# Kernel tuning notes

Hardware: AMD Instinct MI355X
Metric: run time of the kernel (lower is better)

The kernel has to match this reference:

```python
import jax, jax.numpy as jnp
import numpy as np

N, L, S, C, H = 4, 2048, 4096, 256, 8
D = C // H          # head dim = 32
HID = 4 * C         # mlp hidden = 1024
LN_EPS = 1e-5
LA_EPS = 1e-6


def _layer_norm(x, g, b):
    m = x.mean(-1, keepdims=True)
    v = ((x - m) ** 2).mean(-1, keepdims=True)
    return (x - m) * jax.lax.rsqrt(v + LN_EPS) * g + b


def _linear_attention(q, k, v):
    # q: [N,L,H,D], k/v: [N,S,H,D]  (elu feature map linear attention)
    Q = jax.nn.elu(q) + 1.0
    K = jax.nn.elu(k) + 1.0
    v_len = v.shape[1]
    KV = jnp.einsum('nshd,nshv->nhdv', K, v / v_len)
    Z = 1.0 / (jnp.einsum('nlhd,nhd->nlh', Q, K.sum(axis=1)) + LA_EPS)
    return jnp.einsum('nlhd,nhdv,nlh->nlhv', Q, KV, Z) * v_len


def setup_inputs() -> dict:
    key = jax.random.key(0)
    ks = jax.random.split(key, 32)
    f32 = jnp.float32
    w = lambda k, *s: (jax.random.normal(k, s, dtype=f32) * 0.02)
    inp = {
        'tgt': jax.random.normal(ks[0], (N, L, C), dtype=f32),
        'memory': jax.random.normal(ks[1], (N, S, C), dtype=f32),
        'tgt_pos': jax.random.normal(ks[2], (N, L, C), dtype=f32),
        'pos_embed': w(ks[3], 1, S, C),
        # layer norms
        'ln1_g': jnp.ones((C,), f32), 'ln1_b': jnp.zeros((C,), f32),
        'ln2_g': jnp.ones((C,), f32), 'ln2_b': jnp.zeros((C,), f32),
        'ln3_g': jnp.ones((C,), f32), 'ln3_b': jnp.zeros((C,), f32),
        # self-attn projections (stored (in,out))
        'wq': w(ks[4], C, C), 'bq': jnp.zeros((C,), f32),
        'wk': w(ks[5], C, C), 'bk': jnp.zeros((C,), f32),
        'wv': w(ks[6], C, C), 'bv': jnp.zeros((C,), f32),
        'w_merge': w(ks[7], C, C),
        # cross-attn (CCAttention) projections
        'cwq': w(ks[8], C, C), 'cbq': jnp.zeros((C,), f32),
        'cwk': w(ks[9], C, C), 'cbk': jnp.zeros((C,), f32),
        'cwv': w(ks[10], C, C), 'cbv': jnp.zeros((C,), f32),
        'cwo': w(ks[11], C, C), 'cbo': jnp.zeros((C,), f32),
        # mlp (fc1 -> dwconv3x3 -> gelu -> fc2)
        'mw1': w(ks[12], C, HID), 'mb1': jnp.zeros((HID,), f32),
        'dw_k': w(ks[13], HID, 1, 3, 3), 'dw_b': jnp.zeros((HID,), f32),
        'mw2': w(ks[14], HID, C), 'mb2': jnp.zeros((C,), f32),
        'num_points': L,
    }
    return inp


def reference(tgt, memory, tgt_pos, pos_embed,
              ln1_g, ln1_b, ln2_g, ln2_b, ln3_g, ln3_b,
              wq, bq, wk, bk, wv, bv, w_merge,
              cwq, cbq, cwk, cbk, cwv, cbv, cwo, cbo,
              mw1, mb1, dw_k, dw_b, mw2, mb2, num_points):
    n, l, c = tgt.shape
    # ---- self attention (linear attention) ----
    tgt2 = _layer_norm(tgt, ln1_g, ln1_b)
    qk = tgt2 + tgt_pos
    q = (qk @ wq + bq).reshape(n, l, H, D)
    k = (qk @ wk + bk).reshape(n, l, H, D)
    v = (tgt2 @ wv + bv).reshape(n, l, H, D)
    msg = _linear_attention(q, k, v).reshape(n, l, c) @ w_merge
    tgt = tgt + msg  # dropout is identity in eval
    # ---- cross attention (CCAttention, softmax MHA) ----
    tgt2 = _layer_norm(tgt, ln2_g, ln2_b)
    mem = memory + pos_embed
    cq = (tgt2 @ cwq + cbq).reshape(n, l, H, D)
    ck = (mem @ cwk + cbk).reshape(n, -1, H, D)
    cv = (mem @ cwv + cbv).reshape(n, -1, H, D)
    scale = D ** -0.5
    attn = jax.nn.softmax(jnp.einsum('nlhd,nshd->nhls', cq, ck) * scale, axis=-1)
    cmsg = jnp.einsum('nhls,nshd->nlhd', attn, cv).reshape(n, l, c) @ cwo + cbo
    tgt = tgt + cmsg
    # ---- MLP with depthwise conv over (num_points, 1) grid ----
    x = _layer_norm(tgt, ln3_g, ln3_b)
    h = x @ mw1 + mb1                                   # [n,l,HID]
    hi = h.transpose(0, 2, 1).reshape(n, HID, num_points, 1)
    hi = jax.lax.conv_general_dilated(
        hi, dw_k, window_strides=(1, 1), padding=((1, 1), (1, 1)),
        feature_group_count=HID,
        dimension_numbers=('NCHW', 'OIHW', 'NCHW'))
    hi = hi + dw_b[None, :, None, None]
    h = hi.reshape(n, HID, l).transpose(0, 2, 1)
    h = jax.nn.gelu(h, approximate=False)
    mlp_out = h @ mw2 + mb2
    return tgt + mlp_out
```

## Files before the change

### kernel.cpp

```cpp
#include <hip/hip_runtime.h>
#include <hip/hip_bf16.h>
#include <math.h>

#define NB 4
#define LL 2048
#define SS 4096
#define CC 256
#define HH 8
#define DD 32
#define HIDN 1024
#define NSPLIT 4

using bf16 = __hip_bfloat16;
typedef __attribute__((ext_vector_type(8))) short short8;
typedef __attribute__((ext_vector_type(4))) short short4v;
typedef __attribute__((ext_vector_type(4))) float floatx4;

__device__ __forceinline__ float b2f(bf16 x) { return __bfloat162float(x); }
__device__ __forceinline__ short f2bs(float x) {
    bf16 h = __float2bfloat16(x);
    return *(short*)&h;
}
__device__ __forceinline__ short f2bs_fast(float x) {
    return (short)(__float_as_uint(x) >> 16);
}
__device__ __forceinline__ float s2f(short s) {
    bf16 h = *(bf16*)&s;
    return __bfloat162float(h);
}

#if __has_builtin(__builtin_amdgcn_exp2f)
#define EXP2(x) __builtin_amdgcn_exp2f(x)
#else
#define EXP2(x) exp2f(x)
#endif

__device__ __forceinline__ bool probe_f32(const unsigned* p) {
    return p[0] == 0x3F800000u;
}
__device__ __forceinline__ float ldx(const void* p, size_t i, bool f32m) {
    return f32m ? ((const float*)p)[i] : b2f(((const bf16*)p)[i]);
}

struct WPack { const void* p[10]; };

__global__ __launch_bounds__(256)
void wprep_kernel(WPack pk, short* __restrict__ dst, float* __restrict__ zbuf,
                  const unsigned* __restrict__ probe) {
    const int z = blockIdx.z;
    const int tid = threadIdx.x;
    if (z == 10) {
        int idx = (blockIdx.y * 16 + blockIdx.x) * 256 + tid;
        if (idx < 35072) zbuf[idx] = 0.0f;
        return;
    }
    const bool f32m = probe_f32(probe);
    const int K = (z == 9) ? 1024 : 256;
    const int N = (z == 8) ? 1024 : 256;
    const size_t off = (z < 8) ? (size_t)z * 65536 : (z == 8 ? 524288u : 786432u);
    const int k0 = blockIdx.y * 64, n0 = blockIdx.x * 64;
    if (k0 >= K || n0 >= N) return;
    __shared__ float T[64][65];
    const void* src = pk.p[z];
    #pragma unroll
    for (int p = 0; p < 16; ++p) {
        int idx = tid + p * 256;
        int r = idx >> 6, c = idx & 63;
        T[r][c] = ldx(src, (size_t)(k0 + r) * N + n0 + c, f32m);
    }
    __syncthreads();
    short* d = dst + off;
    #pragma unroll
    for (int p = 0; p < 16; ++p) {
        int idx = tid + p * 256;
        int c2 = idx >> 6, r2 = idx & 63;
        d[(size_t)(n0 + c2) * K + k0 + r2] = f2bs(T[r2][c2]);
    }
}

__global__ __launch_bounds__(256)
void ln_kernel(const void* __restrict__ xr, const float* __restrict__ xf,
               const void* __restrict__ g, const void* __restrict__ bta,
               const void* __restrict__ pos,
               short* __restrict__ y, short* __restrict__ y2,
               const unsigned* __restrict__ probe) {
    const bool f32m = probe_f32(probe);
    const int row = blockIdx.x;
    const int c = threadIdx.x;
    const size_t base = (size_t)row * CC;
    float x = xr ? ldx(xr, base + c, f32m) : xf[base + c];
    float a = x, b = x * x;
    #pragma unroll
    for (int off = 32; off; off >>= 1) {
        a += __shfl_down(a, off);
        b += __shfl_down(b, off);
    }
    __shared__ float sa[4], sb[4];
    if ((c & 63) == 0) { sa[c >> 6] = a; sb[c >> 6] = b; }
    __syncthreads();
    float s1 = sa[0] + sa[1] + sa[2] + sa[3];
    float s2 = sb[0] + sb[1] + sb[2] + sb[3];
    float mean = s1 * (1.0f / CC);
    float var = s2 * (1.0f / CC) - mean * mean;
    float inv = rsqrtf(var + 1e-5f);
    float yv = (x - mean) * inv * ldx(g, c, f32m) + ldx(bta, c, f32m);
    y[base + c] = f2bs(yv);
    if (y2) y2[base + c] = f2bs(yv + ldx(pos, base + c, f32m));
}

__global__ __launch_bounds__(256)
void ln_addpos_kernel(const float* __restrict__ xf, const void* __restrict__ g,
                      const void* __restrict__ bta, short* __restrict__ y,
                      const void* __restrict__ mem, const void* __restrict__ pos,
                      short* __restrict__ memout,
                      const unsigned* __restrict__ probe) {
    const bool f32m = probe_f32(probe);
    int row = blockIdx.x;
    const int c = threadIdx.x;
    if (row >= NB * LL) {
        row -= NB * LL;
        const int s = row & (SS - 1);
        memout[(size_t)row * CC + c] =
            f2bs(ldx(mem, (size_t)row * CC + c, f32m) + ldx(pos, (size_t)s * CC + c, f32m));
        return;
    }
    const size_t base = (size_t)row * CC;
    float x = xf[base + c];
    float a = x, b = x * x;
    #pragma unroll
    for (int off = 32; off; off >>= 1) {
        a += __shfl_down(a, off);
        b += __shfl_down(b, off);
    }
    __shared__ float sa[4], sb[4];
    if ((c & 63) == 0) { sa[c >> 6] = a; sb[c >> 6] = b; }
    __syncthreads();
    float s1 = sa[0] + sa[1] + sa[2] + sa[3];
    float s2 = sb[0] + sb[1] + sb[2] + sb[3];
    float mean = s1 * (1.0f / CC);
    float var = s2 * (1.0f / CC) - mean * mean;
    float inv = rsqrtf(var + 1e-5f);
    y[base + c] = f2bs((x - mean) * inv * ldx(g, c, f32m) + ldx(bta, c, f32m));
}

template <int BM, int BN>
__device__ __forceinline__
void gemm_body(const short* __restrict__ A, const short* __restrict__ Bt,
               const void* bias, const void* bias2,
               const float* __restrict__ residF, const void* __restrict__ residR,
               void* Cout, void* Cout2,
               int N, int K, bool f32m, int epi, int outmode, int transc2,
               int bx, int by) {
    constexpr int WM = BM / 2, AI = WM / 16;
    constexpr int WN = BN / 2, BJ = WN / 16;
    constexpr int ACH = (BM == 128) ? 4 : 2;
    constexpr int BCH = (BN == 128) ? 4 : 2;
    __shared__ __attribute__((aligned(16))) short As[BM][72];
    __shared__ __attribute__((aligned(16))) short Bs[BN][72];
    const int tid = threadIdx.x;
    const int ln = tid & 15, quad = (tid >> 4) & 3, w = tid >> 6;
    const int wm = (w & 1) * WM, wn = (w >> 1) * WN;
    const int bm = by * BM, bn = bx * BN;
    const int ar = (BM == 128) ? (tid >> 1) : (tid >> 2);
    const int ac = (BM == 128) ? ((tid & 1) * 32) : ((tid & 3) * 16);
    const int br = (BN == 128) ? (tid >> 1) : (tid >> 2);
    const int bc = (BN == 128) ? ((tid & 1) * 32) : ((tid & 3) * 16);

    short8 pa[ACH], pb[BCH];
    {
        const short* ag = &A[(size_t)(bm + ar) * K + ac];
        #pragma unroll
        for (int t = 0; t < ACH; ++t) pa[t] = *(const short8*)(ag + t * 8);
        const short* bg = &Bt[(size_t)(bn + br) * K + bc];
        #pragma unroll
        for (int t = 0; t < BCH; ++t) pb[t] = *(const short8*)(bg + t * 8);
    }
    floatx4 acc[AI][BJ] = {};
    for (int k0 = 0; k0 < K; k0 += 64) {
        #pragma unroll
        for (int t = 0; t < ACH; ++t) *(short8*)&As[ar][ac + t * 8] = pa[t];
        #pragma unroll
        for (int t = 0; t < BCH; ++t) *(short8*)&Bs[br][bc + t * 8] = pb[t];
        if (k0 + 64 < K) {
            const short* ag = &A[(size_t)(bm + ar) * K + k0 + 64 + ac];
            #pragma unroll
            for (int t = 0; t < ACH; ++t) pa[t] = *(const short8*)(ag + t * 8);
            const short* bg = &Bt[(size_t)(bn + br) * K + k0 + 64 + bc];
            #pragma unroll
            for (int t = 0; t < BCH; ++t) pb[t] = *(const short8*)(bg + t * 8);
        }
        __syncthreads();
        #pragma unroll
        for (int ks = 0; ks < 2; ++ks) {
            short8 af[AI], bf[BJ];
            #pragma unroll
            for (int i = 0; i < AI; ++i)
                af[i] = *(const short8*)&As[wm + i * 16 + ln][ks * 32 + quad * 8];
            #pragma unroll
            for (int j = 0; j < BJ; ++j)
                bf[j] = *(const short8*)&Bs[wn + j * 16 + ln][ks * 32 + quad * 8];
            #pragma unroll
            for (int i = 0; i < AI; ++i)
                #pragma unroll
                for (int j = 0; j < BJ; ++j)
                    acc[i][j] = __builtin_amdgcn_mfma_f32_16x16x32_bf16(af[i], bf[j], acc[i][j], 0, 0, 0);
        }
        __syncthreads();
    }
    #pragma unroll
    for (int i = 0; i < AI; ++i)
        #pragma unroll
        for (int j = 0; j < BJ; ++j) {
            const int gr0 = bm + wm + i * 16 + quad * 4;
            const int gc = bn + wn + j * 16 + ln;
            const bool hi = (Cout2 != nullptr) && (gc >= 256);
            const int col = hi ? gc - 256 : gc;
            const int sN = Cout2 ? 256 : N;
            void* co = hi ? Cout2 : Cout;
            const void* bb = hi ? bias2 : bias;
            float vv[4];
            #pragma unroll
            for (int r = 0; r < 4; ++r) {
                float v = acc[i][j][r];
                if (bb) v += ldx(bb, col, f32m);
                if (epi == 1) v = (v > 0.0f) ? (v + 1.0f) : __expf(v);
                const size_t o = (size_t)(gr0 + r) * sN + col;
                if (residF) v += residF[o];
                if (residR) v += ldx(residR, o, f32m);
                vv[r] = v;
            }
            if (transc2 && hi) {
                const int nb = gr0 >> 12;
                const int s = gr0 & (SS - 1);
                short4v pk4 = {f2bs(vv[0]), f2bs(vv[1]), f2bs(vv[2]), f2bs(vv[3])};
                *(short4v*)&((short*)co)[((size_t)nb * CC + col) * SS + s] = pk4;
            } else {
                #pragma unroll
                for (int r = 0; r < 4; ++r) {
                    const size_t o = (size_t)(gr0 + r) * sN + col;
                    if (outmode == 0) ((float*)co)[o] = vv[r];
                    else if (outmode == 2) ((short*)co)[o] = f2bs(vv[r]);
                    else {
                        if (f32m) ((float*)co)[o] = vv[r];
                        else      ((bf16*)co)[o] = __float2bfloat16(vv[r]);
                    }
                }
            }
        }
}

template <int BM, int BN, int EPI, int OUTMODE, int TRANSC2>
__global__ __launch_bounds__(256)
void gemm_mfma_kernel(const short* __restrict__ A, const short* __restrict__ Bt,
                      const void* __restrict__ bias, const void* __restrict__ bias2,
                      const float* __restrict__ residF, const void* __restrict__ residR,
                      void* __restrict__ Cout, void* __restrict__ Cout2,
                      int M, int N, int K, const unsigned* __restrict__ probe) {
    (void)M;
    gemm_body<BM, BN>(A, Bt, bias, bias2, residF, residR, Cout, Cout2,
                      N, K, probe_f32(probe), EPI, OUTMODE, TRANSC2,
                      blockIdx.x, blockIdx.y);
}

__global__ __launch_bounds__(256)
void gemm_qkv_kernel(const short* __restrict__ qkA, const short* __restrict__ wqkT,
                     const void* bq, const void* bk,
                     float* __restrict__ phiq, float* __restrict__ phik,
                     const short* __restrict__ vA, const short* __restrict__ wvT,
                     const void* bv, float* __restrict__ vout,
                     const unsigned* __restrict__ probe) {
    const bool f32m = probe_f32(probe);
    const bool second = blockIdx.x >= 8;
    gemm_body<64, 64>(second ? vA : qkA,
                      second ? wvT : wqkT,
                      second ? bv : bq,
                      second ? nullptr : bk,
                      nullptr, nullptr,
                      second ? (void*)vout : (void*)phiq,
                      second ? nullptr : (void*)phik,
                      second ? 256 : 512, 256, f32m,
                      second ? 0 : 1, 0, 0,
                      second ? (int)blockIdx.x - 8 : (int)blockIdx.x, blockIdx.y);
}

__global__ __launch_bounds__(256)
void gemm_cqckcv_kernel(const short* __restrict__ lnA, const short* __restrict__ cwqT,
                        const void* cbq, short* __restrict__ cqout,
                        const short* __restrict__ memA, const short* __restrict__ cwkvT,
                        const void* cbk, const void* cbv,
                        short* __restrict__ ckout, short* __restrict__ cvTout,
                        const unsigned* __restrict__ probe) {
    const bool f32m = probe_f32(probe);
    const bool second = blockIdx.x >= 4;
    if (!second && blockIdx.y >= (NB * LL) / 64) return;
    gemm_body<64, 64>(second ? memA : lnA,
                      second ? cwkvT : cwqT,
                      second ? cbk : cbq,
                      second ? cbv : nullptr,
                      nullptr, nullptr,
                      second ? (void*)ckout : (void*)cqout,
                      second ? (void*)cvTout : nullptr,
                      second ? 512 : 256, 256, f32m,
                      0, 2, second ? 1 : 0,
                      second ? (int)blockIdx.x - 4 : (int)blockIdx.x, blockIdx.y);
}

#define KVSPLIT 16
__global__ __launch_bounds__(256)
void linattn_kv_kernel(const float* __restrict__ Kp, const float* __restrict__ Vp,
                       float* __restrict__ KV, float* __restrict__ Ksum) {
    const int h = blockIdx.x, n = blockIdx.y, z = blockIdx.z;
    __shared__ __attribute__((aligned(16))) float Kt[64][33];
    __shared__ __attribute__((aligned(16))) float Vt[64][32];
    const int tid = threadIdx.x;
    const int d = tid >> 3, e0 = (tid & 7) * 4;
    const int sbeg = z * (LL / KVSPLIT), send = sbeg + (LL / KVSPLIT);
    float acc[4] = {}, ks = 0.0f;
    for (int s0 = sbeg; s0 < send; s0 += 64) {
        #pragma unroll
        for (int p = 0; p < 8; ++p) {
            int idx = tid + p * 256;
            int r = idx >> 5, c = idx & 31;
            size_t gaddr = (size_t)((n * LL) + s0 + r) * CC + h * DD + c;
            Kt[r][c] = Kp[gaddr];
            Vt[r][c] = Vp[gaddr];
        }
        __syncthreads();
        for (int s = 0; s < 64; ++s) {
            float kd = Kt[s][d];
            ks += kd;
            float4 v4 = *(const float4*)&Vt[s][e0];
            acc[0] += kd * v4.x; acc[1] += kd * v4.y;
            acc[2] += kd * v4.z; acc[3] += kd * v4.w;
        }
        __syncthreads();
    }
    float* kvp = &KV[(size_t)((n * HH + h) * DD + d) * DD + e0];
    atomicAdd(&kvp[0], acc[0]); atomicAdd(&kvp[1], acc[1]);
    atomicAdd(&kvp[2], acc[2]); atomicAdd(&kvp[3], acc[3]);
    if ((tid & 7) == 0) atomicAdd(&Ksum[(n * HH + h) * DD + d], ks);
}

__global__ __launch_bounds__(256)
void linattn_out_kernel(const float* __restrict__ Qp, const float* __restrict__ KV,
                        const float* __restrict__ Ksum, short* __restrict__ Out) {
    const int lt = blockIdx.x, h = blockIdx.y, n = blockIdx.z;
    __shared__ float KVs[32][33];
    __shared__ float Ks[32];
    __shared__ float Qs[64][33];
    const int tid = threadIdx.x;
    for (int p = 0; p < 4; ++p) {
        int idx = tid + p * 256;
        KVs[idx >> 5][idx & 31] = KV[(size_t)(n * HH + h) * (DD * DD) + idx];
    }
    if (tid < 32) Ks[tid] = Ksum[(n * HH + h) * DD + tid];
    for (int p = 0; p < 8; ++p) {
        int idx = tid + p * 256;
        int r = idx >> 5, c = idx & 31;
        Qs[r][c] = Qp[(size_t)((n * LL) + lt * 64 + r) * CC + h * DD + c];
    }
    __syncthreads();
    const int e = tid & 31;
    for (int ii = 0; ii < 8; ++ii) {
        const int i = (tid >> 5) + ii * 8;
        float num = 0.0f, den = 0.0f;
        for (int d = 0; d < 32; ++d) {
            float q = Qs[i][d];
            num += q * KVs[d][e];
            den += q * Ks[d];
        }
        Out[(size_t)((n * LL) + lt * 64 + i) * CC + h * DD + e] = f2bs(num / (den + 1e-6f));
    }
}

__global__ __launch_bounds__(256)
void flash_mfma_kernel(const short* __restrict__ Q, const short* __restrict__ K,
                       const short* __restrict__ V,
                       float* __restrict__ Of, float* __restrict__ Lp) {
    const int lt = blockIdx.x, h = blockIdx.y;
    const int n = blockIdx.z / NSPLIT, sp = blockIdx.z % NSPLIT;
    const int tid = threadIdx.x;
    const int ln = tid & 15;
    const int quad = (tid >> 4) & 3;
    const int w = tid >> 6;
    const int NT = NB * LL;
    const float qscale = 0.17677669529663687f * 1.4426950408889634f;

    __shared__ __attribute__((aligned(16))) short Ks[2][64][40];
    __shared__ __attribute__((aligned(16))) short Vp[2][32][72];

    short8 bQa, bQb;
    {
        const size_t qrow = (size_t)(n * LL) + lt * 128 + w * 16 + ln;
        short8 qv0 = *(const short8*)&Q[qrow * CC + h * DD + quad * 8];
        short8 qv1 = *(const short8*)&Q[(qrow + 64) * CC + h * DD + quad * 8];
        short t0[8], t1[8];
        #pragma unroll
        for (int j = 0; j < 8; ++j) {
            t0[j] = f2bs(s2f(qv0[j]) * qscale);
            t1[j] = f2bs(s2f(qv1[j]) * qscale);
        }
        bQa = *(short8*)t0;
        bQb = *(short8*)t1;
    }

    const short one_b = (short)0x3F80;
    const short8 ones8 = {one_b, one_b, one_b, one_b, one_b, one_b, one_b, one_b};

    floatx4 o0a = {0.f, 0.f, 0.f, 0.f}, o1a = {0.f, 0.f, 0.f, 0.f};
    floatx4 o2a = {0.f, 0.f, 0.f, 0.f};
    floatx4 o0b = {0.f, 0.f, 0.f, 0.f}, o1b = {0.f, 0.f, 0.f, 0.f};
    floatx4 o2b = {0.f, 0.f, 0.f, 0.f};
    const floatx4 zinit = {-24.f, -24.f, -24.f, -24.f};

    const int r_st = tid >> 2, c0_st = (tid & 3) * 8;
    const int e_st = tid >> 3, m_st = tid & 7;
    const int K32 = (m_st >> 2) * 32;
    const int h4 = ((m_st >> 1) & 1) * 4;
    const int q0s = (2 * m_st) & 3;
    const int slotA = K32 + q0s * 8 + h4;
    const int slotB = K32 + (q0s + 1) * 8 + h4;

    const int sbeg = sp * (SS / NSPLIT);
    constexpr int NIT = (SS / NSPLIT) / 64;

    const short* kptr = &K[(size_t)((n * SS) + sbeg + r_st) * CC + h * DD + c0_st];
    const short* vptr = &V[((size_t)n * CC + h * DD + e_st) * SS + sbeg + m_st * 8];
    short8 kreg = *(const short8*)kptr;
    short8 vreg = *(const short8*)vptr;

    for (int it = 0; it < NIT; ++it) {
        const int buf = it & 1;
        *(short8*)&Ks[buf][r_st][c0_st] = kreg;
        {
            short4v lo = {vreg[0], vreg[1], vreg[2], vreg[3]};
            short4v hi = {vreg[4], vreg[5], vreg[6], vreg[7]};
            *(short4v*)&Vp[buf][e_st][slotA] = lo;
            *(short4v*)&Vp[buf][e_st][slotB] = hi;
        }
        if (it + 1 < NIT) {
            kreg = *(const short8*)(kptr + (size_t)(it + 1) * 64 * CC);
            vreg = *(const short8*)(vptr + (it + 1) * 64);
        }
        __syncthreads();

        floatx4 sa[4], sb[4];
        #pragma unroll
        for (int g = 0; g < 4; ++g) {
            short8 aK = *(const short8*)&Ks[buf][g * 16 + ln][quad * 8];
            sa[g] = __builtin_amdgcn_mfma_f32_16x16x32_bf16(aK, bQa, zinit, 0, 0, 0);
            sb[g] = __builtin_amdgcn_mfma_f32_16x16x32_bf16(aK, bQb, zinit, 0, 0, 0);
        }

        #pragma unroll
        for (int ks = 0; ks < 2; ++ks) {
            union { unsigned u[4]; short8 s8; } ca, cb;
            #pragma unroll
            for (int jj = 0; jj < 4; ++jj) {
                const int j0 = 2 * jj, j1 = 2 * jj + 1;
                float pa0 = EXP2(sa[2 * ks + (j0 >> 2)][j0 & 3]);
                float pa1 = EXP2(sa[2 * ks + (j1 >> 2)][j1 & 3]);
                ca.u[jj] = __builtin_amdgcn_perm(
                    __float_as_uint(pa1), __float_as_uint(pa0), 0x07060302u);
                float pb0 = EXP2(sb[2 * ks + (j0 >> 2)][j0 & 3]);
                float pb1 = EXP2(sb[2 * ks + (j1 >> 2)][j1 & 3]);
                cb.u[jj] = __builtin_amdgcn_perm(
                    __float_as_uint(pb1), __float_as_uint(pb0), 0x07060302u);
            }
            short8 bV0 = *(const short8*)&Vp[buf][ln][ks * 32 + quad * 8];
            short8 bV1 = *(const short8*)&Vp[buf][16 + ln][ks * 32 + quad * 8];
            o0a = __builtin_amdgcn_mfma_f32_16x16x32_bf16(ca.s8, bV0, o0a, 0, 0, 0);
            o1a = __builtin_amdgcn_mfma_f32_16x16x32_bf16(ca.s8, bV1, o1a, 0, 0, 0);
            o2a = __builtin_amdgcn_mfma_f32_16x16x32_bf16(ca.s8, ones8, o2a, 0, 0, 0);
            o0b = __builtin_amdgcn_mfma_f32_16x16x32_bf16(cb.s8, bV0, o0b, 0, 0, 0);
            o1b = __builtin_amdgcn_mfma_f32_16x16x32_bf16(cb.s8, bV1, o1b, 0, 0, 0);
            o2b = __builtin_amdgcn_mfma_f32_16x16x32_bf16(cb.s8, ones8, o2b, 0, 0, 0);
        }
    }

    const int rb_a = lt * 128 + w * 16;
    const int rb_b = rb_a + 64;
    if (ln == 0) {
        #pragma unroll
        for (int r = 0; r < 4; ++r) {
            Lp[((size_t)sp * NT + (size_t)n * LL + rb_a + quad * 4 + r) * HH + h] = o2a[r];
            Lp[((size_t)sp * NT + (size_t)n * LL + rb_b + quad * 4 + r) * HH + h] = o2b[r];
        }
    }
    #pragma unroll
    for (int r = 0; r < 4; ++r) {
        {
            const size_t row = (size_t)n * LL + rb_a + quad * 4 + r;
            float* o = &Of[((size_t)sp * NT + row) * CC + h * DD];
            o[ln] = o0a[r];
            o[16 + ln] = o1a[r];
        }
        {
            const size_t row = (size_t)n * LL + rb_b + quad * 4 + r;
            float* o = &Of[((size_t)sp * NT + row) * CC + h * DD];
            o[ln] = o0b[r];
            o[16 + ln] = o1b[r];
        }
    }
}

__global__ __launch_bounds__(256)
void flash_merge_kernel(const float* __restrict__ Of, const float* __restrict__ Lp,
                        short* __restrict__ O) {
    const int row = blockIdx.x, c = threadIdx.x, h = c >> 5;
    const size_t NT = (size_t)NB * LL;
    float l = 0.0f, v = 0.0f;
    #pragma unroll
    for (int sp = 0; sp < NSPLIT; ++sp) {
        l += Lp[((size_t)sp * NT + row) * HH + h];
        v += Of[((size_t)sp * NT + row) * CC + c];
    }
    O[(size_t)row * CC + c] = f2bs(v / l);
}

__global__ __launch_bounds__(256)
void dwconv_gelu_kernel(const short* __restrict__ H1, const void* __restrict__ wk,
                        const void* __restrict__ wb, short* __restrict__ H2,
                        const unsigned* __restrict__ probe) {
    const bool f32m = probe_f32(probe);
    const int row = blockIdx.x;
    const int l = row & (LL - 1);
    const int c0 = threadIdx.x * 4;
    const short* cur = &H1[(size_t)row * HIDN + c0];
    short4v xc = *(const short4v*)cur;
    short4v xm = {}, xp = {};
    if (l > 0)      xm = *(const short4v*)(cur - HIDN);
    if (l < LL - 1) xp = *(const short4v*)(cur + HIDN);
    short r[4];
    #pragma unroll
    for (int j = 0; j < 4; ++j) {
        int ch = c0 + j;
        float wm = ldx(wk, ch * 9 + 1, f32m);
        float w0 = ldx(wk, ch * 9 + 4, f32m);
        float wp = ldx(wk, ch * 9 + 7, f32m);
        float v = s2f(xm[j]) * wm + s2f(xc[j]) * w0 + s2f(xp[j]) * wp + ldx(wb, ch, f32m);
        r[j] = f2bs(0.5f * v * (1.0f + erff(v * 0.70710678118654752f)));
    }
    short4v out = {r[0], r[1], r[2], r[3]};
    *(short4v*)&H2[(size_t)row * HIDN + c0] = out;
}

extern "C" void kernel_launch(void* const* d_in, const int* in_sizes, int n_in,
                              void* d_out, int out_size, void* d_ws, size_t ws_size,
                              hipStream_t stream) {
    const void* tgt      = d_in[0];
    const void* memory   = d_in[1];
    const void* tgt_pos  = d_in[2];
    const void* pos_emb  = d_in[3];
    const void* ln1_g = d_in[4],  *ln1_b = d_in[5];
    const void* ln2_g = d_in[6],  *ln2_b = d_in[7];
    const void* ln3_g = d_in[8],  *ln3_b = d_in[9];
    const void* wq = d_in[10], *bq = d_in[11];
    const void* wk = d_in[12], *bk = d_in[13];
    const void* wv = d_in[14], *bv = d_in[15];
    const void* w_merge = d_in[16];
    const void* cwq = d_in[17], *cbq = d_in[18];
    const void* cwk = d_in[19], *cbk = d_in[20];
    const void* cwv = d_in[21], *cbv = d_in[22];
    const void* cwo = d_in[23], *cbo = d_in[24];
    const void* mw1 = d_in[25], *mb1 = d_in[26];
    const void* dw_k = d_in[27], *dw_b = d_in[28];
    const void* mw2 = d_in[29], *mb2 = d_in[30];
    const unsigned* probe = (const unsigned*)d_in[4];

    char* w = (char*)d_ws;
    const size_t MB = 1024 * 1024;
    short* lnout_b = (short*)(w + 0 * MB);
    short* qk_b    = (short*)(w + 4 * MB);
    float* Tbuf    = (float*)(w + 8 * MB);
    float* phiq    = (float*)(w + 16 * MB);
    float* phik    = (float*)(w + 24 * MB);
    float* vbuf    = (float*)(w + 32 * MB);
    float* KVb     = (float*)(w + 40 * MB);
    float* Ksb     = (float*)(w + 40 * MB + 131072);
    float* Ofb     = (float*)(w + 16 * MB);
    float* Lpb     = (float*)(w + 48 * MB);
    short* cqbuf   = (short*)(w + 49 * MB);
    short* membuf  = (short*)(w + 53 * MB);
    short* ckbuf   = (short*)(w + 61 * MB);
    short* cvT     = (short*)(w + 69 * MB);
    short* flashO  = (short*)(w + 77 * MB);
    short* wT      = (short*)(w + 81 * MB);
    short* H1      = (short*)(w + 16 * MB);
    short* H2      = (short*)(w + 32 * MB);

    short* wqT  = wT + 0 * 65536;
    short* wvT  = wT + 2 * 65536;
    short* wmT  = wT + 3 * 65536;
    short* cwqT = wT + 4 * 65536;
    short* cwkT = wT + 5 * 65536;
    short* cwoT = wT + 7 * 65536;
    short* mw1T = wT + 524288;
    short* mw2T = wT + 786432;

    const int NT = NB * LL;
    const int NS = NB * SS;
    const dim3 blk(256);

    WPack pk;
    pk.p[0] = wq;  pk.p[1] = wk;  pk.p[2] = wv;  pk.p[3] = w_merge;
    pk.p[4] = cwq; pk.p[5] = cwk; pk.p[6] = cwv; pk.p[7] = cwo;
    pk.p[8] = mw1; pk.p[9] = mw2;
    wprep_kernel<<<dim3(16, 16, 11), blk, 0, stream>>>(pk, wT, KVb, probe);

    ln_kernel<<<NT, blk, 0, stream>>>(tgt, nullptr, ln1_g, ln1_b, tgt_pos, lnout_b, qk_b, probe);
    gemm_qkv_kernel<<<dim3(12, NT / 64), blk, 0, stream>>>(
        qk_b, wqT, bq, bk, phiq, phik, lnout_b, wvT, bv, vbuf, probe);
    linattn_kv_kernel<<<dim3(HH, NB, KVSPLIT), blk, 0, stream>>>(phik, vbuf, KVb, Ksb);
    linattn_out_kernel<<<dim3(LL / 64, HH, NB), blk, 0, stream>>>(phiq, KVb, Ksb, (short*)vbuf);
    gemm_mfma_kernel<64, 64, 0, 0, 0><<<dim3(4, NT / 64), blk, 0, stream>>>(
        (short*)vbuf, wmT, nullptr, nullptr, nullptr, tgt, Tbuf, nullptr, NT, CC, CC, probe);

    ln_addpos_kernel<<<NT + NS, blk, 0, stream>>>(
        Tbuf, ln2_g, ln2_b, lnout_b, memory, pos_emb, membuf, probe);
    gemm_cqckcv_kernel<<<dim3(12, NS / 64), blk, 0, stream>>>(
        lnout_b, cwqT, cbq, cqbuf, membuf, cwkT, cbk, cbv, ckbuf, cvT, probe);
    flash_mfma_kernel<<<dim3(LL / 128, HH, NB * NSPLIT), blk, 0, stream>>>(
        cqbuf, ckbuf, cvT, Ofb, Lpb);
    flash_merge_kernel<<<NT, blk, 0, stream>>>(Ofb, Lpb, flashO);
    gemm_mfma_kernel<64, 64, 0, 0, 0><<<dim3(4, NT / 64), blk, 0, stream>>>(
        flashO, cwoT, cbo, nullptr, Tbuf, nullptr, Tbuf, nullptr, NT, CC, CC, probe);

    ln_kernel<<<NT, blk, 0, stream>>>(nullptr, Tbuf, ln3_g, ln3_b, nullptr, lnout_b, nullptr, probe);
    gemm_mfma_kernel<64, 64, 0, 2, 0><<<dim3(16, NT / 64), blk, 0, stream>>>(
        lnout_b, mw1T, mb1, nullptr, nullptr, nullptr, H1, nullptr, NT, HIDN, CC, probe);
    dwconv_gelu_kernel<<<NT, blk, 0, stream>>>(H1, dw_k, dw_b, H2, probe);
    gemm_mfma_kernel<64, 64, 0, 1, 0><<<dim3(4, NT / 64), blk, 0, stream>>>(
        H2, mw2T, mb2, nullptr, Tbuf, nullptr, d_out, nullptr, NT, CC, HIDN, probe);

    (void)in_sizes; (void)n_in; (void)out_size; (void)ws_size;
}
```

Measured before the change: 413.0 us.

## Vectorize layer norms per wave, double-buffer GEMM LDS, split flash launch

The layer-norm kernels now process one row per 64-lane wave with 4-wide vector loads and stores, and reduce with xor shuffles instead of a shared-memory block reduction. The generic GEMM body double-buffers its LDS tiles and drops the trailing barrier in each k-iteration. The flash attention launch is split into two half-grid launches using a z offset. Together these aim to cut memory instruction count, barrier cost and LDS stalls, at the cost of twice the LDS per GEMM block and one extra kernel launch.

```diff
diff --git a/kernel.cpp b/kernel.cpp
--- a/kernel.cpp
+++ b/kernel.cpp
@@ -41,6 +41,16 @@
 __device__ __forceinline__ float ldx(const void* p, size_t i, bool f32m) {
     return f32m ? ((const float*)p)[i] : b2f(((const bf16*)p)[i]);
 }
+__device__ __forceinline__ void ldx4(const void* p, size_t i, bool f32m, float* x) {
+    if (f32m) {
+        float4 v = *(const float4*)((const float*)p + i);
+        x[0] = v.x; x[1] = v.y; x[2] = v.z; x[3] = v.w;
+    } else {
+        short4v s = *(const short4v*)((const short*)p + i);
+        #pragma unroll
+        for (int j = 0; j < 4; ++j) x[j] = s2f(s[j]);
+    }
+}
 
 struct WPack { const void* p[10]; };
 
@@ -85,27 +95,42 @@
                short* __restrict__ y, short* __restrict__ y2,
                const unsigned* __restrict__ probe) {
     const bool f32m = probe_f32(probe);
-    const int row = blockIdx.x;
-    const int c = threadIdx.x;
+    const int w = threadIdx.x >> 6, lane = threadIdx.x & 63;
+    const int row = blockIdx.x * 4 + w;
+    const int c0 = lane * 4;
     const size_t base = (size_t)row * CC;
-    float x = xr ? ldx(xr, base + c, f32m) : xf[base + c];
-    float a = x, b = x * x;
-    #pragma unroll
-    for (int off = 32; off; off >>= 1) {
-        a += __shfl_down(a, off);
-        b += __shfl_down(b, off);
-    }
-    __shared__ float sa[4], sb[4];
-    if ((c & 63) == 0) { sa[c >> 6] = a; sb[c >> 6] = b; }
-    __syncthreads();
-    float s1 = sa[0] + sa[1] + sa[2] + sa[3];
-    float s2 = sb[0] + sb[1] + sb[2] + sb[3];
-    float mean = s1 * (1.0f / CC);
-    float var = s2 * (1.0f / CC) - mean * mean;
-    float inv = rsqrtf(var + 1e-5f);
-    float yv = (x - mean) * inv * ldx(g, c, f32m) + ldx(bta, c, f32m);
-    y[base + c] = f2bs(yv);
-    if (y2) y2[base + c] = f2bs(yv + ldx(pos, base + c, f32m));
+    float x[4];
+    if (xr) ldx4(xr, base + c0, f32m, x);
+    else {
+        float4 v = *(const float4*)(xf + base + c0);
+        x[0] = v.x; x[1] = v.y; x[2] = v.z; x[3] = v.w;
+    }
+    float a = x[0] + x[1] + x[2] + x[3];
+    float b = x[0]*x[0] + x[1]*x[1] + x[2]*x[2] + x[3]*x[3];
+    #pragma unroll
+    for (int off = 1; off < 64; off <<= 1) {
+        a += __shfl_xor(a, off);
+        b += __shfl_xor(b, off);
+    }
+    const float mean = a * (1.0f / CC);
+    const float var = b * (1.0f / CC) - mean * mean;
+    const float inv = rsqrtf(var + 1e-5f);
+    float yv[4];
+    short r[4];
+    #pragma unroll
+    for (int j = 0; j < 4; ++j) {
+        yv[j] = (x[j] - mean) * inv * ldx(g, c0 + j, f32m) + ldx(bta, c0 + j, f32m);
+        r[j] = f2bs(yv[j]);
+    }
+    *(short4v*)&y[base + c0] = short4v{r[0], r[1], r[2], r[3]};
+    if (y2) {
+        float pz[4];
+        ldx4(pos, base + c0, f32m, pz);
+        short r2[4];
+        #pragma unroll
+        for (int j = 0; j < 4; ++j) r2[j] = f2bs(yv[j] + pz[j]);
+        *(short4v*)&y2[base + c0] = short4v{r2[0], r2[1], r2[2], r2[3]};
+    }
 }
 
 __global__ __launch_bounds__(256)
@@ -115,32 +140,39 @@
                       short* __restrict__ memout,
                       const unsigned* __restrict__ probe) {
     const bool f32m = probe_f32(probe);
-    int row = blockIdx.x;
-    const int c = threadIdx.x;
+    const int w = threadIdx.x >> 6, lane = threadIdx.x & 63;
+    int row = blockIdx.x * 4 + w;
+    const int c0 = lane * 4;
     if (row >= NB * LL) {
         row -= NB * LL;
         const int s = row & (SS - 1);
-        memout[(size_t)row * CC + c] =
-            f2bs(ldx(mem, (size_t)row * CC + c, f32m) + ldx(pos, (size_t)s * CC + c, f32m));
+        float m[4], p[4];
+        ldx4(mem, (size_t)row * CC + c0, f32m, m);
+        ldx4(pos, (size_t)s * CC + c0, f32m, p);
+        short r[4];
+        #pragma unroll
+        for (int j = 0; j < 4; ++j) r[j] = f2bs(m[j] + p[j]);
+        *(short4v*)&memout[(size_t)row * CC + c0] = short4v{r[0], r[1], r[2], r[3]};
         return;
     }
     const size_t base = (size_t)row * CC;
-    float x = xf[base + c];
-    float a = x, b = x * x;
-    #pragma unroll
-    for (int off = 32; off; off >>= 1) {
-        a += __shfl_down(a, off);
-        b += __shfl_down(b, off);
-    }
-    __shared__ float sa[4], sb[4];
-    if ((c & 63) == 0) { sa[c >> 6] = a; sb[c >> 6] = b; }
-    __syncthreads();
-    float s1 = sa[0] + sa[1] + sa[2] + sa[3];
-    float s2 = sb[0] + sb[1] + sb[2] + sb[3];
-    float mean = s1 * (1.0f / CC);
-    float var = s2 * (1.0f / CC) - mean * mean;
-    float inv = rsqrtf(var + 1e-5f);
-    y[base + c] = f2bs((x - mean) * inv * ldx(g, c, f32m) + ldx(bta, c, f32m));
+    float4 v = *(const float4*)(xf + base + c0);
+    float x[4] = {v.x, v.y, v.z, v.w};
+    float a = x[0] + x[1] + x[2] + x[3];
+    float b = x[0]*x[0] + x[1]*x[1] + x[2]*x[2] + x[3]*x[3];
+    #pragma unroll
+    for (int off = 1; off < 64; off <<= 1) {
+        a += __shfl_xor(a, off);
+        b += __shfl_xor(b, off);
+    }
+    const float mean = a * (1.0f / CC);
+    const float var = b * (1.0f / CC) - mean * mean;
+    const float inv = rsqrtf(var + 1e-5f);
+    short r[4];
+    #pragma unroll
+    for (int j = 0; j < 4; ++j)
+        r[j] = f2bs((x[j] - mean) * inv * ldx(g, c0 + j, f32m) + ldx(bta, c0 + j, f32m));
+    *(short4v*)&y[base + c0] = short4v{r[0], r[1], r[2], r[3]};
 }
 
 template <int BM, int BN>
@@ -155,8 +187,8 @@
     constexpr int WN = BN / 2, BJ = WN / 16;
     constexpr int ACH = (BM == 128) ? 4 : 2;
     constexpr int BCH = (BN == 128) ? 4 : 2;
-    __shared__ __attribute__((aligned(16))) short As[BM][72];
-    __shared__ __attribute__((aligned(16))) short Bs[BN][72];
+    __shared__ __attribute__((aligned(16))) short As[2][BM][72];
+    __shared__ __attribute__((aligned(16))) short Bs[2][BN][72];
     const int tid = threadIdx.x;
     const int ln = tid & 15, quad = (tid >> 4) & 3, w = tid >> 6;
     const int wm = (w & 1) * WM, wn = (w >> 1) * WN;
@@ -176,16 +208,19 @@
         for (int t = 0; t < BCH; ++t) pb[t] = *(const short8*)(bg + t * 8);
     }
     floatx4 acc[AI][BJ] = {};
-    for (int k0 = 0; k0 < K; k0 += 64) {
-        #pragma unroll
-        for (int t = 0; t < ACH; ++t) *(short8*)&As[ar][ac + t * 8] = pa[t];
-        #pragma unroll
-        for (int t = 0; t < BCH; ++t) *(short8*)&Bs[br][bc + t * 8] = pb[t];
-        if (k0 + 64 < K) {
-            const short* ag = &A[(size_t)(bm + ar) * K + k0 + 64 + ac];
+    const int NK = K >> 6;
+    for (int it = 0; it < NK; ++it) {
+        const int buf = it & 1;
+        #pragma unroll
+        for (int t = 0; t < ACH; ++t) *(short8*)&As[buf][ar][ac + t * 8] = pa[t];
+        #pragma unroll
+        for (int t = 0; t < BCH; ++t) *(short8*)&Bs[buf][br][bc + t * 8] = pb[t];
+        if (it + 1 < NK) {
+            const int k1 = (it + 1) << 6;
+            const short* ag = &A[(size_t)(bm + ar) * K + k1 + ac];
             #pragma unroll
             for (int t = 0; t < ACH; ++t) pa[t] = *(const short8*)(ag + t * 8);
-            const short* bg = &Bt[(size_t)(bn + br) * K + k0 + 64 + bc];
+            const short* bg = &Bt[(size_t)(bn + br) * K + k1 + bc];
             #pragma unroll
             for (int t = 0; t < BCH; ++t) pb[t] = *(const short8*)(bg + t * 8);
         }
@@ -195,17 +230,16 @@
             short8 af[AI], bf[BJ];
             #pragma unroll
             for (int i = 0; i < AI; ++i)
-                af[i] = *(const short8*)&As[wm + i * 16 + ln][ks * 32 + quad * 8];
+                af[i] = *(const short8*)&As[buf][wm + i * 16 + ln][ks * 32 + quad * 8];
             #pragma unroll
             for (int j = 0; j < BJ; ++j)
-                bf[j] = *(const short8*)&Bs[wn + j * 16 + ln][ks * 32 + quad * 8];
+                bf[j] = *(const short8*)&Bs[buf][wn + j * 16 + ln][ks * 32 + quad * 8];
             #pragma unroll
             for (int i = 0; i < AI; ++i)
                 #pragma unroll
                 for (int j = 0; j < BJ; ++j)
                     acc[i][j] = __builtin_amdgcn_mfma_f32_16x16x32_bf16(af[i], bf[j], acc[i][j], 0, 0, 0);
         }
-        __syncthreads();
     }
     #pragma unroll
     for (int i = 0; i < AI; ++i)
@@ -376,9 +410,10 @@
 __global__ __launch_bounds__(256)
 void flash_mfma_kernel(const short* __restrict__ Q, const short* __restrict__ K,
                        const short* __restrict__ V,
-                       float* __restrict__ Of, float* __restrict__ Lp) {
+                       float* __restrict__ Of, float* __restrict__ Lp, int zoff) {
     const int lt = blockIdx.x, h = blockIdx.y;
-    const int n = blockIdx.z / NSPLIT, sp = blockIdx.z % NSPLIT;
+    const int z = blockIdx.z + zoff;
+    const int n = z / NSPLIT, sp = z % NSPLIT;
     const int tid = threadIdx.x;
     const int ln = tid & 15;
     const int quad = (tid >> 4) & 3;
@@ -608,7 +643,7 @@
     pk.p[8] = mw1; pk.p[9] = mw2;
     wprep_kernel<<<dim3(16, 16, 11), blk, 0, stream>>>(pk, wT, KVb, probe);
 
-    ln_kernel<<<NT, blk, 0, stream>>>(tgt, nullptr, ln1_g, ln1_b, tgt_pos, lnout_b, qk_b, probe);
+    ln_kernel<<<NT / 4, blk, 0, stream>>>(tgt, nullptr, ln1_g, ln1_b, tgt_pos, lnout_b, qk_b, probe);
     gemm_qkv_kernel<<<dim3(12, NT / 64), blk, 0, stream>>>(
         qk_b, wqT, bq, bk, phiq, phik, lnout_b, wvT, bv, vbuf, probe);
     linattn_kv_kernel<<<dim3(HH, NB, KVSPLIT), blk, 0, stream>>>(phik, vbuf, KVb, Ksb);
@@ -616,17 +651,19 @@
     gemm_mfma_kernel<64, 64, 0, 0, 0><<<dim3(4, NT / 64), blk, 0, stream>>>(
         (short*)vbuf, wmT, nullptr, nullptr, nullptr, tgt, Tbuf, nullptr, NT, CC, CC, probe);
 
-    ln_addpos_kernel<<<NT + NS, blk, 0, stream>>>(
+    ln_addpos_kernel<<<(NT + NS) / 4, blk, 0, stream>>>(
         Tbuf, ln2_g, ln2_b, lnout_b, memory, pos_emb, membuf, probe);
     gemm_cqckcv_kernel<<<dim3(12, NS / 64), blk, 0, stream>>>(
         lnout_b, cwqT, cbq, cqbuf, membuf, cwkT, cbk, cbv, ckbuf, cvT, probe);
-    flash_mfma_kernel<<<dim3(LL / 128, HH, NB * NSPLIT), blk, 0, stream>>>(
-        cqbuf, ckbuf, cvT, Ofb, Lpb);
+    flash_mfma_kernel<<<dim3(LL / 128, HH, NB * NSPLIT / 2), blk, 0, stream>>>(
+        cqbuf, ckbuf, cvT, Ofb, Lpb, 0);
+    flash_mfma_kernel<<<dim3(LL / 128, HH, NB * NSPLIT / 2), blk, 0, stream>>>(
+        cqbuf, ckbuf, cvT, Ofb, Lpb, NB * NSPLIT / 2);
     flash_merge_kernel<<<NT, blk, 0, stream>>>(Ofb, Lpb, flashO);
     gemm_mfma_kernel<64, 64, 0, 0, 0><<<dim3(4, NT / 64), blk, 0, stream>>>(
         flashO, cwoT, cbo, nullptr, Tbuf, nullptr, Tbuf, nullptr, NT, CC, CC, probe);
 
-    ln_kernel<<<NT, blk, 0, stream>>>(nullptr, Tbuf, ln3_g, ln3_b, nullptr, lnout_b, nullptr, probe);
+    ln_kernel<<<NT / 4, blk, 0, stream>>>(nullptr, Tbuf, ln3_g, ln3_b, nullptr, lnout_b, nullptr, probe);
     gemm_mfma_kernel<64, 64, 0, 2, 0><<<dim3(16, NT / 64), blk, 0, stream>>>(
         lnout_b, mw1T, mb1, nullptr, nullptr, nullptr, H1, nullptr, NT, HIDN, CC, probe);
     dwconv_gelu_kernel<<<NT, blk, 0, stream>>>(H1, dw_k, dw_b, H2, probe);
```

Result: no change. 410.4 us (-0.6%).
